# Kernel optimization log

Hardware: AMD Instinct MI355X
Metric: run time of the kernel (lower is better)

The kernel has to match this reference:

```python
import jax, jax.numpy as jnp
import numpy as np

G, FO, FI = 8, 64, 64   # n_group, fo, fi
N_ITER = 3
B, H, W = 32, 64, 64


def setup_inputs() -> dict:
    key = jax.random.key(0)
    k1, k2, k3 = jax.random.split(key, 3)
    x = jax.random.normal(k1, (B, G * FI, H, W), jnp.float32)
    # kaiming_normal on [fo*g, fi, 1, 1] -> std = sqrt(2/fi); stored as [g, fo, fi]
    weight = jax.random.normal(k2, (G, FO, FI), jnp.float32) * np.float32(np.sqrt(2.0 / FI))
    bias = jax.random.normal(k3, (FO,), jnp.float32)
    return {"x": x, "weight": weight, "bias": bias}


def reference(x, weight, bias):
    b, c, h, w = x.shape
    g, fo, fi = weight.shape
    # grouped 1x1 conv: split channels into g groups of fi, contract each with its [fo, fi] block
    xr = x.reshape(b, g, fi, h, w)
    con = jnp.einsum('bgihw,goi->bgohw', xr, weight)  # [B, g, fo, H, W]
    beta = jnp.zeros((1, g, 1, 1, 1), dtype=x.dtype)
    for i in range(N_ITER):
        alpha = jax.nn.sigmoid(beta)
        v = jnp.sum(alpha * con, axis=1, keepdims=True)      # [B, 1, fo, H, W]
        if i == N_ITER - 1:
            return v[:, 0] + bias[None, :, None, None]       # [B, fo, H, W]
        beta = beta + jnp.sum(v * con, axis=2, keepdims=True)  # [B, g, 1, H, W]
```

## Files before the change

### kernel.cpp

```cpp
#include <hip/hip_runtime.h>


#define NG 8
#define NFO 64
#define NFI 64
#define NB 32
#define NH 64
#define NW 64
#define HW (NH * NW)

typedef float v2f __attribute__((ext_vector_type(2)));

__device__ __forceinline__ void stage_piece(const float* gsrc, float* ldst) {
    __builtin_amdgcn_global_load_lds(
        (const __attribute__((address_space(1))) void*)gsrc,
        (__attribute__((address_space(3))) void*)ldst, 16, 0, 0);
}

__global__ __launch_bounds__(256) void conv_kernel(
    const float* __restrict__ x, const float* __restrict__ weight,
    float* __restrict__ con)
{
    const int tid = threadIdx.x;
    const int p = tid & 63;
    const int q = __builtin_amdgcn_readfirstlane(tid >> 6);

    const int id = blockIdx.x;
    const int t = id & 31;
    const int g = (id >> 5) & 7;
    const int b = id >> 8;

    __shared__ __align__(16) float smem[8192];

    const float* xg = x + ((size_t)b * (NG * NFI) + (size_t)g * NFI) * HW + t * 128;

    const float* gs = xg + (size_t)(p >> 5) * HW + (size_t)(p & 31) * 4;
#pragma unroll
    for (int k = 0; k < 8; ++k) {
        const int chpair = q * 8 + k;
        stage_piece(gs + (size_t)(2 * chpair) * HW, smem + chpair * 256);
    }
    asm volatile("s_waitcnt vmcnt(0)" ::: "memory");
    __builtin_amdgcn_s_barrier();

    v2f acc[16];
#pragma unroll
    for (int f = 0; f < 16; ++f) acc[f] = (v2f){0.f, 0.f};

    const float* wq = weight + ((size_t)g * NFO + (size_t)q * 16) * NFI;

#pragma unroll
    for (int chb = 0; chb < 8; ++chb) {
        v2f xr[8];
#pragma unroll
        for (int j = 0; j < 8; ++j)
            xr[j] = *(const v2f*)&smem[(chb * 8 + j) * 128 + 2 * p];
#pragma unroll
        for (int f = 0; f < 16; ++f) {
            const float* wr = wq + (size_t)f * NFI + chb * 8;
#pragma unroll
            for (int j = 0; j < 8; ++j) {
                const float w = wr[j];
                acc[f] = __builtin_elementwise_fma((v2f){w, w}, xr[j], acc[f]);
            }
        }
    }

    float* crow = con + (((size_t)(b * NG + g) * NFO + (size_t)q * 16)) * HW
                      + t * 128 + 2 * p;
#pragma unroll
    for (int f = 0; f < 16; ++f)
        *(v2f*)(crow + (size_t)f * HW) = acc[f];
}

__global__ __launch_bounds__(512) void route_kernel(
    const float* __restrict__ con, const float* __restrict__ bias,
    float* __restrict__ out)
{
    const int tid = threadIdx.x;
    const int p = tid & 63;
    const int q = __builtin_amdgcn_readfirstlane(tid >> 6);

    const int id = blockIdx.x;
    const int t = id & 63;
    const int b = id >> 6;

    __shared__ float pbuf[8][8][64];
    __shared__ float alphaS[8][64];
    __shared__ float betaS[8][64];

    float c[8][8];
#pragma unroll
    for (int g = 0; g < 8; ++g) {
        const float* cr = con + (((size_t)(b * NG + g) * NFO + (size_t)q * 8)) * HW
                              + t * 64 + p;
#pragma unroll
        for (int f = 0; f < 8; ++f) c[g][f] = cr[(size_t)f * HW];
    }

    float v[8];

#pragma unroll
    for (int f = 0; f < 8; ++f) {
        float s = c[0][f];
#pragma unroll
        for (int g = 1; g < 8; ++g) s += c[g][f];
        v[f] = 0.5f * s;
    }
#pragma unroll
    for (int g = 0; g < 8; ++g) {
        float s = 0.f;
#pragma unroll
        for (int f = 0; f < 8; ++f) s = fmaf(v[f], c[g][f], s);
        pbuf[q][g][p] = s;
    }
    __syncthreads();
    {
        const int gg = tid >> 6, pp = tid & 63;
        float bs = 0.f;
#pragma unroll
        for (int w = 0; w < 8; ++w) bs += pbuf[w][gg][pp];
        betaS[gg][pp] = bs;
        alphaS[gg][pp] = 1.f / (1.f + __expf(-bs));
    }
    __syncthreads();

    float a[8];
#pragma unroll
    for (int g = 0; g < 8; ++g) a[g] = alphaS[g][p];
#pragma unroll
    for (int f = 0; f < 8; ++f) {
        float s = 0.f;
#pragma unroll
        for (int g = 0; g < 8; ++g) s = fmaf(a[g], c[g][f], s);
        v[f] = s;
    }
#pragma unroll
    for (int g = 0; g < 8; ++g) {
        float s = 0.f;
#pragma unroll
        for (int f = 0; f < 8; ++f) s = fmaf(v[f], c[g][f], s);
        pbuf[q][g][p] = s;
    }
    __syncthreads();
    {
        const int gg = tid >> 6, pp = tid & 63;
        float bs = betaS[gg][pp];
#pragma unroll
        for (int w = 0; w < 8; ++w) bs += pbuf[w][gg][pp];
        alphaS[gg][pp] = 1.f / (1.f + __expf(-bs));
    }
    __syncthreads();

#pragma unroll
    for (int g = 0; g < 8; ++g) a[g] = alphaS[g][p];

    const float* bq = bias + q * 8;
    float* orow = out + (((size_t)b * NFO + (size_t)q * 8) * NH + t) * NW + p;
#pragma unroll
    for (int f = 0; f < 8; ++f) {
        float s = bq[f];
#pragma unroll
        for (int g = 0; g < 8; ++g) s = fmaf(a[g], c[g][f], s);
        orow[(size_t)f * HW] = s;
    }
}

__global__ __launch_bounds__(512, 2) void dynrout_kernel(
    const float* __restrict__ x, const float* __restrict__ weight,
    const float* __restrict__ bias, float* __restrict__ out)
{
    const int tid = threadIdx.x;
    const int p = tid & 63;
    const int q = __builtin_amdgcn_readfirstlane(tid >> 6);

    const int wg = blockIdx.x;
    const int b = wg >> 6;
    const int h = wg & 63;

    const float* xcol = x + (size_t)b * (NG * NFI) * HW + (size_t)h * NW + p;

    float con[8][8];

#pragma unroll
    for (int g = 0; g < 8; ++g) {
        const float* xg = xcol + (size_t)g * NFI * HW;
        const float* wgb = weight + ((size_t)g * NFO + (size_t)q * 8) * NFI;

        v2f acc[8];
#pragma unroll
        for (int f = 0; f < 8; ++f) acc[f] = (v2f){0.f, 0.f};

#pragma unroll
        for (int sub = 0; sub < 4; ++sub) {
            v2f xr[8];
#pragma unroll
            for (int j = 0; j < 8; ++j) {
                xr[j].x = xg[(size_t)(sub * 16 + 2 * j) * HW];
                xr[j].y = xg[(size_t)(sub * 16 + 2 * j + 1) * HW];
            }
#pragma unroll
            for (int f = 0; f < 8; ++f) {
                const float* wr = wgb + f * NFI + sub * 16;
#pragma unroll
                for (int j = 0; j < 8; ++j) {
                    const v2f wv = *(const v2f*)(wr + 2 * j);
                    acc[f] = __builtin_elementwise_fma(wv, xr[j], acc[f]);
                }
            }
        }
#pragma unroll
        for (int f = 0; f < 8; ++f) con[g][f] = acc[f].x + acc[f].y;

        __builtin_amdgcn_s_barrier();
    }

    __shared__ float pbuf[8][8][64];
    __shared__ float alphaS[8][64];
    __shared__ float betaS[8][64];

    float v[8];
#pragma unroll
    for (int f = 0; f < 8; ++f) {
        float s = con[0][f];
#pragma unroll
        for (int g = 1; g < 8; ++g) s += con[g][f];
        v[f] = 0.5f * s;
    }
#pragma unroll
    for (int g = 0; g < 8; ++g) {
        float s = 0.f;
#pragma unroll
        for (int f = 0; f < 8; ++f) s = fmaf(v[f], con[g][f], s);
        pbuf[q][g][p] = s;
    }
    __syncthreads();
    {
        const int gg = tid >> 6, pp = tid & 63;
        float bs = 0.f;
#pragma unroll
        for (int w = 0; w < 8; ++w) bs += pbuf[w][gg][pp];
        betaS[gg][pp] = bs;
        alphaS[gg][pp] = 1.f / (1.f + __expf(-bs));
    }
    __syncthreads();

    float a[8];
#pragma unroll
    for (int g = 0; g < 8; ++g) a[g] = alphaS[g][p];
#pragma unroll
    for (int f = 0; f < 8; ++f) {
        float s = 0.f;
#pragma unroll
        for (int g = 0; g < 8; ++g) s = fmaf(a[g], con[g][f], s);
        v[f] = s;
    }
#pragma unroll
    for (int g = 0; g < 8; ++g) {
        float s = 0.f;
#pragma unroll
        for (int f = 0; f < 8; ++f) s = fmaf(v[f], con[g][f], s);
        pbuf[q][g][p] = s;
    }
    __syncthreads();
    {
        const int gg = tid >> 6, pp = tid & 63;
        float bs = betaS[gg][pp];
#pragma unroll
        for (int w = 0; w < 8; ++w) bs += pbuf[w][gg][pp];
        alphaS[gg][pp] = 1.f / (1.f + __expf(-bs));
    }
    __syncthreads();

#pragma unroll
    for (int g = 0; g < 8; ++g) a[g] = alphaS[g][p];

    const float* bq = bias + q * 8;
    float* orow = out + (((size_t)b * NFO + (size_t)q * 8) * NH + h) * NW + p;
#pragma unroll
    for (int f = 0; f < 8; ++f) {
        float s = bq[f];
#pragma unroll
        for (int g = 0; g < 8; ++g) s = fmaf(a[g], con[g][f], s);
        orow[(size_t)f * HW] = s;
    }
}

extern "C" void kernel_launch(void* const* d_in, const int* in_sizes, int n_in,
                              void* d_out, int out_size, void* d_ws, size_t ws_size,
                              hipStream_t stream) {
    const float* x      = (const float*)d_in[0];
    const float* weight = (const float*)d_in[1];
    const float* bias   = (const float*)d_in[2];
    float* out = (float*)d_out;

    const size_t need = (size_t)NB * NG * NFO * HW * sizeof(float);
    if (d_ws != nullptr && ws_size >= need) {
        float* con = (float*)d_ws;
        conv_kernel<<<dim3(NB * NG * 32), dim3(256), 0, stream>>>(x, weight, con);
        route_kernel<<<dim3(NB * 64), dim3(512), 0, stream>>>(con, bias, out);
    } else {
        dynrout_kernel<<<dim3(NB * NH), dim3(512), 0, stream>>>(x, weight, bias, out);
    }
}
```

Baseline: 547.6 us.

## Store intermediate conv output in fp16 and double-buffer conv tiles

The grouped-conv intermediate is written and read as half precision instead of fp32, halving the dominant intermediate memory traffic between the two kernels. The conv kernel now processes four 64-pixel tiles per block with double-buffered async LDS staging to overlap loads with compute. The routing kernel uses 256 threads with 16 output features per wave. The fp16 intermediate adds rounding error to the routing iterations.

New measurement: 468.9 us. 14.4% less time.

```diff
diff --git a/kernel.cpp b/kernel.cpp
--- a/kernel.cpp
+++ b/kernel.cpp
@@ -19,62 +19,84 @@
 
 __global__ __launch_bounds__(256) void conv_kernel(
     const float* __restrict__ x, const float* __restrict__ weight,
-    float* __restrict__ con)
+    _Float16* __restrict__ con)
 {
     const int tid = threadIdx.x;
     const int p = tid & 63;
     const int q = __builtin_amdgcn_readfirstlane(tid >> 6);
 
     const int id = blockIdx.x;
-    const int t = id & 31;
-    const int g = (id >> 5) & 7;
-    const int b = id >> 8;
+    const int quad = id & 15;
+    const int g = (id >> 4) & 7;
+    const int b = id >> 7;
 
     __shared__ __align__(16) float smem[8192];
 
-    const float* xg = x + ((size_t)b * (NG * NFI) + (size_t)g * NFI) * HW + t * 128;
-
-    const float* gs = xg + (size_t)(p >> 5) * HW + (size_t)(p & 31) * 4;
-#pragma unroll
-    for (int k = 0; k < 8; ++k) {
-        const int chpair = q * 8 + k;
-        stage_piece(gs + (size_t)(2 * chpair) * HW, smem + chpair * 256);
-    }
-    asm volatile("s_waitcnt vmcnt(0)" ::: "memory");
-    __builtin_amdgcn_s_barrier();
-
-    v2f acc[16];
-#pragma unroll
-    for (int f = 0; f < 16; ++f) acc[f] = (v2f){0.f, 0.f};
+    const float* xg = x + ((size_t)b * (NG * NFI) + (size_t)g * NFI) * HW;
+    const size_t laneoff = (size_t)(p >> 4) * HW + (size_t)(p & 15) * 4;
+
+#define STAGE_TILE(t, bb)                                                     \
+    {                                                                         \
+        _Pragma("unroll")                                                     \
+        for (int cc = 0; cc < 4; ++cc) {                                      \
+            const int chb = q * 16 + cc * 4;                                  \
+            stage_piece(xg + (size_t)(t) * 64 + (size_t)chb * HW + laneoff,   \
+                        smem + (bb) * 4096 + chb * 64);                       \
+        }                                                                     \
+    }
+
+    STAGE_TILE(quad * 4 + 0, 0);
+    STAGE_TILE(quad * 4 + 1, 1);
 
     const float* wq = weight + ((size_t)g * NFO + (size_t)q * 16) * NFI;
 
 #pragma unroll
-    for (int chb = 0; chb < 8; ++chb) {
-        v2f xr[8];
-#pragma unroll
-        for (int j = 0; j < 8; ++j)
-            xr[j] = *(const v2f*)&smem[(chb * 8 + j) * 128 + 2 * p];
-#pragma unroll
-        for (int f = 0; f < 16; ++f) {
-            const float* wr = wq + (size_t)f * NFI + chb * 8;
-#pragma unroll
-            for (int j = 0; j < 8; ++j) {
-                const float w = wr[j];
-                acc[f] = __builtin_elementwise_fma((v2f){w, w}, xr[j], acc[f]);
+    for (int tt = 0; tt < 4; ++tt) {
+        if (tt < 3) asm volatile("s_waitcnt vmcnt(4)" ::: "memory");
+        else        asm volatile("s_waitcnt vmcnt(0)" ::: "memory");
+        __builtin_amdgcn_s_barrier();
+
+        const float* buf = smem + (tt & 1) * 4096;
+
+        v2f acc[16];
+#pragma unroll
+        for (int f = 0; f < 16; ++f) acc[f] = (v2f){0.f, 0.f};
+
+#pragma unroll
+        for (int ib = 0; ib < 8; ++ib) {
+            v2f xq[4];
+#pragma unroll
+            for (int j = 0; j < 4; ++j) {
+                xq[j].x = buf[(ib * 8 + 2 * j) * 64 + p];
+                xq[j].y = buf[(ib * 8 + 2 * j + 1) * 64 + p];
+            }
+#pragma unroll
+            for (int f = 0; f < 16; ++f) {
+                const float* wr = wq + (size_t)f * NFI + ib * 8;
+#pragma unroll
+                for (int j = 0; j < 4; ++j) {
+                    const v2f wv = *(const v2f*)(wr + 2 * j);
+                    acc[f] = __builtin_elementwise_fma(wv, xq[j], acc[f]);
+                }
             }
         }
-    }
-
-    float* crow = con + (((size_t)(b * NG + g) * NFO + (size_t)q * 16)) * HW
-                      + t * 128 + 2 * p;
-#pragma unroll
-    for (int f = 0; f < 16; ++f)
-        *(v2f*)(crow + (size_t)f * HW) = acc[f];
-}
-
-__global__ __launch_bounds__(512) void route_kernel(
-    const float* __restrict__ con, const float* __restrict__ bias,
+
+        const int t = quad * 4 + tt;
+        _Float16* crow = con + (((size_t)(b * NG + g) * NFO + (size_t)q * 16)) * HW
+                             + (size_t)t * 64 + p;
+#pragma unroll
+        for (int f = 0; f < 16; ++f)
+            crow[(size_t)f * HW] = (_Float16)(acc[f].x + acc[f].y);
+
+        __builtin_amdgcn_s_barrier();
+
+        if (tt < 2) STAGE_TILE(quad * 4 + tt + 2, tt & 1);
+    }
+#undef STAGE_TILE
+}
+
+__global__ __launch_bounds__(256) void route_kernel(
+    const _Float16* __restrict__ con, const float* __restrict__ bias,
     float* __restrict__ out)
 {
     const int tid = threadIdx.x;
@@ -85,23 +107,23 @@
     const int t = id & 63;
     const int b = id >> 6;
 
-    __shared__ float pbuf[8][8][64];
+    __shared__ float pbuf[4][8][64];
     __shared__ float alphaS[8][64];
     __shared__ float betaS[8][64];
 
-    float c[8][8];
-#pragma unroll
-    for (int g = 0; g < 8; ++g) {
-        const float* cr = con + (((size_t)(b * NG + g) * NFO + (size_t)q * 8)) * HW
-                              + t * 64 + p;
-#pragma unroll
-        for (int f = 0; f < 8; ++f) c[g][f] = cr[(size_t)f * HW];
-    }
-
-    float v[8];
-
-#pragma unroll
-    for (int f = 0; f < 8; ++f) {
+    float c[8][16];
+#pragma unroll
+    for (int g = 0; g < 8; ++g) {
+        const _Float16* cr = con + (((size_t)(b * NG + g) * NFO + (size_t)q * 16)) * HW
+                                 + (size_t)t * 64 + p;
+#pragma unroll
+        for (int f = 0; f < 16; ++f) c[g][f] = (float)cr[(size_t)f * HW];
+    }
+
+    float v[16];
+
+#pragma unroll
+    for (int f = 0; f < 16; ++f) {
         float s = c[0][f];
 #pragma unroll
         for (int g = 1; g < 8; ++g) s += c[g][f];
@@ -111,15 +133,14 @@
     for (int g = 0; g < 8; ++g) {
         float s = 0.f;
 #pragma unroll
-        for (int f = 0; f < 8; ++f) s = fmaf(v[f], c[g][f], s);
+        for (int f = 0; f < 16; ++f) s = fmaf(v[f], c[g][f], s);
         pbuf[q][g][p] = s;
     }
     __syncthreads();
-    {
-        const int gg = tid >> 6, pp = tid & 63;
-        float bs = 0.f;
-#pragma unroll
-        for (int w = 0; w < 8; ++w) bs += pbuf[w][gg][pp];
+    for (int k = tid; k < 512; k += 256) {
+        const int gg = k >> 6, pp = k & 63;
+        const float bs = pbuf[0][gg][pp] + pbuf[1][gg][pp] +
+                         pbuf[2][gg][pp] + pbuf[3][gg][pp];
         betaS[gg][pp] = bs;
         alphaS[gg][pp] = 1.f / (1.f + __expf(-bs));
     }
@@ -129,7 +150,7 @@
 #pragma unroll
     for (int g = 0; g < 8; ++g) a[g] = alphaS[g][p];
 #pragma unroll
-    for (int f = 0; f < 8; ++f) {
+    for (int f = 0; f < 16; ++f) {
         float s = 0.f;
 #pragma unroll
         for (int g = 0; g < 8; ++g) s = fmaf(a[g], c[g][f], s);
@@ -139,15 +160,15 @@
     for (int g = 0; g < 8; ++g) {
         float s = 0.f;
 #pragma unroll
-        for (int f = 0; f < 8; ++f) s = fmaf(v[f], c[g][f], s);
+        for (int f = 0; f < 16; ++f) s = fmaf(v[f], c[g][f], s);
         pbuf[q][g][p] = s;
     }
     __syncthreads();
-    {
-        const int gg = tid >> 6, pp = tid & 63;
-        float bs = betaS[gg][pp];
-#pragma unroll
-        for (int w = 0; w < 8; ++w) bs += pbuf[w][gg][pp];
+    for (int k = tid; k < 512; k += 256) {
+        const int gg = k >> 6, pp = k & 63;
+        const float bs = betaS[gg][pp] +
+                         pbuf[0][gg][pp] + pbuf[1][gg][pp] +
+                         pbuf[2][gg][pp] + pbuf[3][gg][pp];
         alphaS[gg][pp] = 1.f / (1.f + __expf(-bs));
     }
     __syncthreads();
@@ -155,10 +176,10 @@
 #pragma unroll
     for (int g = 0; g < 8; ++g) a[g] = alphaS[g][p];
 
-    const float* bq = bias + q * 8;
-    float* orow = out + (((size_t)b * NFO + (size_t)q * 8) * NH + t) * NW + p;
-#pragma unroll
-    for (int f = 0; f < 8; ++f) {
+    const float* bq = bias + q * 16;
+    float* orow = out + (((size_t)b * NFO + (size_t)q * 16) * NH + t) * NW + p;
+#pragma unroll
+    for (int f = 0; f < 16; ++f) {
         float s = bq[f];
 #pragma unroll
         for (int g = 0; g < 8; ++g) s = fmaf(a[g], c[g][f], s);
@@ -294,11 +315,11 @@
     const float* bias   = (const float*)d_in[2];
     float* out = (float*)d_out;
 
-    const size_t need = (size_t)NB * NG * NFO * HW * sizeof(float);
+    const size_t need = (size_t)NB * NG * NFO * HW * sizeof(_Float16);
     if (d_ws != nullptr && ws_size >= need) {
-        float* con = (float*)d_ws;
-        conv_kernel<<<dim3(NB * NG * 32), dim3(256), 0, stream>>>(x, weight, con);
-        route_kernel<<<dim3(NB * 64), dim3(512), 0, stream>>>(con, bias, out);
+        _Float16* con = (_Float16*)d_ws;
+        conv_kernel<<<dim3(NB * NG * 16), dim3(256), 0, stream>>>(x, weight, con);
+        route_kernel<<<dim3(NB * 64), dim3(256), 0, stream>>>(con, bias, out);
     } else {
         dynrout_kernel<<<dim3(NB * NH), dim3(512), 0, stream>>>(x, weight, bias, out);
     }
```
